# Kernel tuning notes

Hardware: AMD Instinct MI355X
Metric: run time of the kernel (lower is better)

Reference implementation:

```python
import jax, jax.numpy as jnp
import numpy as np


def _conv1x1(W, x):
    # W: [out, in], x: [B, in, D, H, W] -> [B, out, D, H, W]
    return jnp.einsum('oc,bcdhw->bodhw', W, x)


def _maxpool2(x):
    # 2x2x2 max pool, stride 2, over the last three (spatial) dims
    return jax.lax.reduce_window(x, -jnp.inf, jax.lax.max,
                                 (1, 1, 2, 2, 2), (1, 1, 2, 2, 2), 'VALID')


def setup_inputs() -> dict:
    key = jax.random.key(0)
    ks = jax.random.split(key, 5)
    B, C, D, H, W = 4, 256, 24, 24, 24
    Cq = C // 8
    x = jax.random.normal(ks[0], (B, C, D, H, W), dtype=jnp.float32)
    Wf = jax.random.normal(ks[1], (Cq, C), dtype=jnp.float32) * (C ** -0.5)
    Wg = jax.random.normal(ks[2], (Cq, C), dtype=jnp.float32) * (C ** -0.5)
    Wh = jax.random.normal(ks[3], (Cq, C), dtype=jnp.float32) * (C ** -0.5)
    Wv = jax.random.normal(ks[4], (C, Cq), dtype=jnp.float32) * (Cq ** -0.5)
    gamma = jnp.ones((), dtype=jnp.float32)
    return {"x": x, "Wf": Wf, "Wg": Wg, "Wh": Wh, "Wv": Wv, "gamma": gamma}


def reference(x, Wf, Wg, Wh, Wv, gamma):
    B, C, D, H, W = x.shape
    Cq = Wf.shape[0]
    N = D * H * W          # query length
    M = N // 8

    f = _conv1x1(Wf, x).reshape(B, Cq, N)                 # [B, Cq, N]
    g = _maxpool2(_conv1x1(Wg, x)).reshape(B, Cq, M)      # [B, Cq, M]
    h = _maxpool2(_conv1x1(Wh, x)).reshape(B, Cq, M)      # [B, Cq, M]

    scores = jnp.einsum('bcn,bcm->bnm', f, g)             # [B, N, M]
    beta = jax.nn.softmax(scores, axis=-1)
    o = jnp.einsum('bcm,bnm->bcn', h, beta)               # [B, Cq, N]
    o = _conv1x1(Wv, o.reshape(B, Cq, D, H, W))           # [B, C, D, H, W]
    return gamma * o + x
```

## Files before the change

### kernel.cpp

```cpp
#include <hip/hip_runtime.h>

#define B 4
#define C 256
#define CQ 32
#define NN 13824
#define MM 1728
#define MS 12

typedef __attribute__((ext_vector_type(8))) short short8;
typedef __attribute__((ext_vector_type(4))) float float4_;
typedef __attribute__((ext_vector_type(16))) float floatx16;

static __device__ inline unsigned rne_bf16(float x) {
  unsigned u = __float_as_uint(x);
  u += 0x7FFFu + ((u >> 16) & 1u);
  return u >> 16;
}

__global__ __launch_bounds__(256) void wcvt_kernel(
    const float* __restrict__ Wf, const float* __restrict__ Wg,
    const float* __restrict__ Wh, const float* __restrict__ Wv,
    unsigned short* __restrict__ W16c, unsigned short* __restrict__ Whv,
    unsigned short* __restrict__ Wlv) {
  const int i = blockIdx.x * 256 + threadIdx.x;
  if (i < 24576) {
    const int kk = i & 7;
    const int rest = i >> 3;
    const int m = rest % 96;
    const int r = rest / 96;
    const int kq = r & 3;
    const int ch = r >> 2;
    const int k = ch * 32 + kq * 8 + kk;
    const float* Wr = (m < 32) ? (Wf + m * C) : (m < 64) ? (Wg + (m - 32) * C)
                                                         : (Wh + (m - 64) * C);
    W16c[i] = (unsigned short)rne_bf16(Wr[k]);
  } else {
    const int j = i - 24576;
    const float v = Wv[j];
    const unsigned h = rne_bf16(v);
    Whv[j] = (unsigned short)h;
    Wlv[j] = (unsigned short)rne_bf16(v - __uint_as_float(h << 16));
  }
}

#define LOADX(SET, CH)                                                        \
  do {                                                                        \
    const float* xp = xbase + (size_t)((CH)*32) * NN;                         \
    _Pragma("unroll") for (int it = 0; it < 2; ++it) {                        \
      _Pragma("unroll") for (int kk = 0; kk < 8; ++kk)                        \
          vx[SET][it][kk] = xp[(size_t)((sh * 2 + it) * 8 + kk) * NN];        \
    }                                                                         \
  } while (0)

#define PACKX(SET, BUF)                                                       \
  do {                                                                        \
    _Pragma("unroll") for (int it = 0; it < 2; ++it) {                        \
      const int kq = sh * 2 + it;                                             \
      *reinterpret_cast<uint4*>(&xls[BUF][kq][sn][0]) = make_uint4(           \
          rne_bf16(vx[SET][it][0]) | (rne_bf16(vx[SET][it][1]) << 16),        \
          rne_bf16(vx[SET][it][2]) | (rne_bf16(vx[SET][it][3]) << 16),        \
          rne_bf16(vx[SET][it][4]) | (rne_bf16(vx[SET][it][5]) << 16),        \
          rne_bf16(vx[SET][it][6]) | (rne_bf16(vx[SET][it][7]) << 16));       \
    }                                                                         \
  } while (0)

#define LOADW(CH)                                                             \
  do {                                                                        \
    const uint4* src = reinterpret_cast<const uint4*>(W16c + (size_t)(CH)*3072); \
    wr0 = src[t];                                                             \
    if (t < 128) wr1 = src[256 + t];                                          \
  } while (0)

#define STOREW(BUF)                                                           \
  do {                                                                        \
    uint4* dst = reinterpret_cast<uint4*>(&wls[BUF][0][0][0]);                \
    dst[t] = wr0;                                                             \
    if (t < 128) dst[256 + t] = wr1;                                          \
  } while (0)

#define COMPUTE(BUF)                                                          \
  do {                                                                        \
    _Pragma("unroll") for (int ks = 0; ks < 2; ++ks) {                        \
      const int kq = ks * 2 + hi;                                             \
      const short8 bfr =                                                      \
          *reinterpret_cast<const short8*>(&xls[BUF][kq][w * 32 + col][0]);   \
      const short8 a0 = *reinterpret_cast<const short8*>(&wls[BUF][kq][col][0]);      \
      const short8 a1 = *reinterpret_cast<const short8*>(&wls[BUF][kq][32 + col][0]); \
      const short8 a2 = *reinterpret_cast<const short8*>(&wls[BUF][kq][64 + col][0]); \
      accf = __builtin_amdgcn_mfma_f32_32x32x16_bf16(a0, bfr, accf, 0, 0, 0); \
      accg = __builtin_amdgcn_mfma_f32_32x32x16_bf16(a1, bfr, accg, 0, 0, 0); \
      acch = __builtin_amdgcn_mfma_f32_32x32x16_bf16(a2, bfr, acch, 0, 0, 0); \
    }                                                                         \
  } while (0)

__global__ __launch_bounds__(256) void proj_mfma(
    const float* __restrict__ x, const unsigned short* __restrict__ W16c,
    unsigned short* __restrict__ f16, unsigned short* __restrict__ g16,
    unsigned short* __restrict__ h16) {
  __shared__ __align__(16) unsigned short xls[2][4][128][8];
  __shared__ __align__(16) unsigned short wls[2][4][96][8];
  const int blk = blockIdx.x;
  const int b = blk / 108;
  const int n0 = (blk - b * 108) * 128;
  const int t = threadIdx.x;
  const int w = t >> 6, lane = t & 63;
  const int col = lane & 31, hi = lane >> 5;
  const int sn = t & 127, sh = t >> 7;

  floatx16 accf = {0}, accg = {0}, acch = {0};
  const float* xbase = x + ((size_t)b * C) * NN + n0 + sn;
  float vx[2][2][8];
  uint4 wr0, wr1;

  LOADX(0, 0);
  PACKX(0, 0);
  LOADW(0);
  STOREW(0);
  LOADX(1, 1);
  __syncthreads();

#pragma unroll
  for (int ch = 0; ch < 8; ++ch) {
    const int buf = ch & 1;
    if (ch + 1 < 8) LOADW(ch + 1);
    if (ch + 2 < 8) {
      if (buf == 0) LOADX(0, ch + 2); else LOADX(1, ch + 2);
    }
    COMPUTE(buf);
    if (ch + 1 < 8) {
      if (buf == 0) PACKX(1, 1); else PACKX(0, 0);
      STOREW(buf ^ 1);
      __syncthreads();
    }
  }

  const int n = n0 + w * 32 + col;
  {
    unsigned short* fp = f16 + ((size_t)b * NN + n) * 32 + hi * 4;
#pragma unroll
    for (int rp = 0; rp < 8; ++rp) {
      const int m = (rp & 1) * 2 + 8 * (rp >> 1);
      *reinterpret_cast<unsigned*>(fp + m) =
          rne_bf16(accf[rp * 2]) | (rne_bf16(accf[rp * 2 + 1]) << 16);
    }
  }
  unsigned short* gp = g16 + (size_t)b * CQ * NN + n;
  unsigned short* hp = h16 + (size_t)b * CQ * NN + n;
#pragma unroll
  for (int r = 0; r < 16; ++r) {
    const int c = (r & 3) + 8 * (r >> 2) + 4 * hi;
    gp[(size_t)c * NN] = (unsigned short)rne_bf16(accg[r]);
    hp[(size_t)c * NN] = (unsigned short)rne_bf16(acch[r]);
  }
}

__global__ __launch_bounds__(256) void pool_kernel(
    const unsigned short* __restrict__ g16, const unsigned short* __restrict__ h16,
    unsigned short* __restrict__ gt16, unsigned short* __restrict__ ht16) {
  int i = blockIdx.x * 256 + threadIdx.x;
  const int c = i & 31;
  const int rest = i >> 5;
  const int m = rest % MM;
  const int b = rest / MM;
  const int wq = m % MS;
  const int hq = (m / MS) % MS;
  const int dq = m / (MS * MS);
  const size_t base = ((size_t)b * CQ + c) * NN +
                      (2 * dq) * 576 + (2 * hq) * 24 + (2 * wq);
  auto mx2 = [](unsigned u) {
    return fmaxf(__uint_as_float(u << 16), __uint_as_float(u & 0xFFFF0000u));
  };
  const unsigned short* pg = g16 + base;
  const unsigned short* ph = h16 + base;
  float vg = fmaxf(fmaxf(mx2(*(const unsigned*)(pg)),
                         mx2(*(const unsigned*)(pg + 24))),
                   fmaxf(mx2(*(const unsigned*)(pg + 576)),
                         mx2(*(const unsigned*)(pg + 600))));
  float vh = fmaxf(fmaxf(mx2(*(const unsigned*)(ph)),
                         mx2(*(const unsigned*)(ph + 24))),
                   fmaxf(mx2(*(const unsigned*)(ph + 576)),
                         mx2(*(const unsigned*)(ph + 600))));
  gt16[((size_t)b * MM + m) * 32 + c] = (unsigned short)(__float_as_uint(vg) >> 16);
  ht16[((size_t)b * 32 + c) * MM + m] = (unsigned short)(__float_as_uint(vh) >> 16);
}

__global__ __launch_bounds__(256, 4) void attn_kernel(
    const unsigned short* __restrict__ f16, const unsigned short* __restrict__ gt,
    const unsigned short* __restrict__ ht, const float* __restrict__ x,
    const unsigned short* __restrict__ Whv, const unsigned short* __restrict__ Wlv,
    const float* __restrict__ gamma, float* __restrict__ out) {
  __shared__ __align__(16) unsigned short sm[16896];
  const int blk = blockIdx.x;
  const int b = blk / 216;
  const int n0 = (blk - b * 216) * 64;
  const int t = threadIdx.x;
  const int w = t >> 6, L = t & 63, Q = L >> 4, col = L & 15;

  unsigned short* fls = sm;
  unsigned short* g0 = sm + 2560;
  unsigned short* g1 = sm + 5120;
  unsigned short* h0 = sm + 7680;
  unsigned short* h1 = sm + 9984;
  unsigned short* Pls = sm + 12288 + w * 1152;

  {
    const unsigned short* fsrc = f16 + ((size_t)(b * NN + n0)) * 32;
    *reinterpret_cast<uint4*>(fls + (t >> 2) * 40 + (t & 3) * 8) =
        *reinterpret_cast<const uint4*>(fsrc + t * 8);
  }
  const unsigned short* gsrc = gt + (size_t)b * MM * 32;
  const unsigned short* hsrc = ht + (size_t)b * 32 * MM;
  const int gk = t >> 2, gseg = t & 3;
  const int hc = t >> 3, hseg = t & 7;
  *reinterpret_cast<uint4*>(g0 + gk * 40 + gseg * 8) =
      *reinterpret_cast<const uint4*>(gsrc + gk * 32 + gseg * 8);
  *reinterpret_cast<uint4*>(h0 + hc * 72 + hseg * 8) =
      *reinterpret_cast<const uint4*>(hsrc + (size_t)hc * MM + hseg * 8);
  __syncthreads();

  const short8 fB = *reinterpret_cast<const short8*>(fls + (w * 16 + col) * 40 + Q * 8);

  float4_ acc0 = {0.f, 0.f, 0.f, 0.f}, acc1 = {0.f, 0.f, 0.f, 0.f};
  float l = 0.f;

  for (int ch = 0; ch < 27; ++ch) {
    unsigned short* gcur = (ch & 1) ? g1 : g0;
    unsigned short* hcur = (ch & 1) ? h1 : h0;
    uint4 gnx, hnx;
    if (ch < 26) {
      const int k0 = (ch + 1) * 64;
      gnx = *reinterpret_cast<const uint4*>(gsrc + (size_t)(k0 + gk) * 32 + gseg * 8);
      hnx = *reinterpret_cast<const uint4*>(hsrc + (size_t)hc * MM + k0 + hseg * 8);
    }
    float4_ sc[4];
#pragma unroll
    for (int T = 0; T < 4; ++T) {
      const short8 gA =
          *reinterpret_cast<const short8*>(gcur + (T * 16 + col) * 40 + Q * 8);
      float4_ z = {0.f, 0.f, 0.f, 0.f};
      sc[T] = __builtin_amdgcn_mfma_f32_16x16x32_bf16(gA, fB, z, 0, 0, 0);
    }
#pragma unroll
    for (int T = 0; T < 4; ++T) {
      const float p0 = __expf(sc[T][0] - 30.f);
      const float p1 = __expf(sc[T][1] - 30.f);
      const float p2 = __expf(sc[T][2] - 30.f);
      const float p3 = __expf(sc[T][3] - 30.f);
      l += (p0 + p1) + (p2 + p3);
      unsigned short* pw = Pls + col * 72 + T * 16 + Q * 4;
      *reinterpret_cast<uint2*>(pw) =
          make_uint2(rne_bf16(p0) | (rne_bf16(p1) << 16),
                     rne_bf16(p2) | (rne_bf16(p3) << 16));
    }
#pragma unroll
    for (int ks = 0; ks < 2; ++ks) {
      const short8 pA =
          *reinterpret_cast<const short8*>(Pls + col * 72 + ks * 32 + Q * 8);
      const short8 hB0 =
          *reinterpret_cast<const short8*>(hcur + col * 72 + ks * 32 + Q * 8);
      const short8 hB1 =
          *reinterpret_cast<const short8*>(hcur + (16 + col) * 72 + ks * 32 + Q * 8);
      acc0 = __builtin_amdgcn_mfma_f32_16x16x32_bf16(pA, hB0, acc0, 0, 0, 0);
      acc1 = __builtin_amdgcn_mfma_f32_16x16x32_bf16(pA, hB1, acc1, 0, 0, 0);
    }
    if (ch < 26) {
      unsigned short* gnb = (ch & 1) ? g0 : g1;
      unsigned short* hnb = (ch & 1) ? h0 : h1;
      *reinterpret_cast<uint4*>(gnb + gk * 40 + gseg * 8) = gnx;
      *reinterpret_cast<uint4*>(hnb + hc * 72 + hseg * 8) = hnx;
    }
    __syncthreads();
  }

  l += __shfl_xor(l, 16);
  l += __shfl_xor(l, 32);
  float* ols = reinterpret_cast<float*>(sm);
#pragma unroll
  for (int r = 0; r < 4; ++r) {
    const float linv = 1.f / __shfl(l, Q * 4 + r);
    const int nl = w * 16 + Q * 4 + r;
    ols[nl * 33 + col] = acc0[r] * linv;
    ols[nl * 33 + 16 + col] = acc1[r] * linv;
  }
  __syncthreads();

  const int colA = L & 31, hiA = L >> 5;
  const float gm = gamma[0];
  short8 Bf[2][2];
#pragma unroll
  for (int nt = 0; nt < 2; ++nt) {
#pragma unroll
    for (int ks = 0; ks < 2; ++ks) {
      const float* p = &ols[(nt * 32 + colA) * 33 + ks * 16 + hiA * 8];
      uint4 uu;
      uu.x = rne_bf16(p[0]) | (rne_bf16(p[1]) << 16);
      uu.y = rne_bf16(p[2]) | (rne_bf16(p[3]) << 16);
      uu.z = rne_bf16(p[4]) | (rne_bf16(p[5]) << 16);
      uu.w = rne_bf16(p[6]) | (rne_bf16(p[7]) << 16);
      Bf[nt][ks] = *reinterpret_cast<short8*>(&uu);
    }
  }
#pragma unroll
  for (int tt = 0; tt < 2; ++tt) {
    const int ct = w + tt * 4;
    const int ca = ct * 32 + colA;
    const short8 Ah0 = *reinterpret_cast<const short8*>(Whv + ca * 32 + hiA * 8);
    const short8 Ah1 = *reinterpret_cast<const short8*>(Whv + ca * 32 + 16 + hiA * 8);
    const short8 Al0 = *reinterpret_cast<const short8*>(Wlv + ca * 32 + hiA * 8);
    const short8 Al1 = *reinterpret_cast<const short8*>(Wlv + ca * 32 + 16 + hiA * 8);
    floatx16 ac0 = {0}, ac1 = {0};
    ac0 = __builtin_amdgcn_mfma_f32_32x32x16_bf16(Ah0, Bf[0][0], ac0, 0, 0, 0);
    ac0 = __builtin_amdgcn_mfma_f32_32x32x16_bf16(Ah1, Bf[0][1], ac0, 0, 0, 0);
    ac0 = __builtin_amdgcn_mfma_f32_32x32x16_bf16(Al0, Bf[0][0], ac0, 0, 0, 0);
    ac0 = __builtin_amdgcn_mfma_f32_32x32x16_bf16(Al1, Bf[0][1], ac0, 0, 0, 0);
    ac1 = __builtin_amdgcn_mfma_f32_32x32x16_bf16(Ah0, Bf[1][0], ac1, 0, 0, 0);
    ac1 = __builtin_amdgcn_mfma_f32_32x32x16_bf16(Ah1, Bf[1][1], ac1, 0, 0, 0);
    ac1 = __builtin_amdgcn_mfma_f32_32x32x16_bf16(Al0, Bf[1][0], ac1, 0, 0, 0);
    ac1 = __builtin_amdgcn_mfma_f32_32x32x16_bf16(Al1, Bf[1][1], ac1, 0, 0, 0);
#pragma unroll
    for (int nt = 0; nt < 2; ++nt) {
      const floatx16 av = nt ? ac1 : ac0;
      const int n = n0 + nt * 32 + colA;
      const float* xp = x + ((size_t)b * C + ct * 32 + 4 * hiA) * NN + n;
      float* op = out + ((size_t)b * C + ct * 32 + 4 * hiA) * NN + n;
      float xv[16];
#pragma unroll
      for (int r = 0; r < 16; ++r)
        xv[r] = xp[(size_t)((r & 3) + 8 * (r >> 2)) * NN];
#pragma unroll
      for (int r = 0; r < 16; ++r)
        op[(size_t)((r & 3) + 8 * (r >> 2)) * NN] = gm * av[r] + xv[r];
    }
  }
}

extern "C" void kernel_launch(void* const* d_in, const int* in_sizes, int n_in,
                              void* d_out, int out_size, void* d_ws, size_t ws_size,
                              hipStream_t stream) {
  const float* x     = (const float*)d_in[0];
  const float* Wf    = (const float*)d_in[1];
  const float* Wg    = (const float*)d_in[2];
  const float* Wh    = (const float*)d_in[3];
  const float* Wv    = (const float*)d_in[4];
  const float* gamma = (const float*)d_in[5];
  float* out = (float*)d_out;
  float* ws = (float*)d_ws;

  unsigned short* f16  = (unsigned short*)ws;
  unsigned short* g16  = (unsigned short*)(ws + 884736);
  unsigned short* h16  = (unsigned short*)(ws + 1769472);
  unsigned short* Whv  = (unsigned short*)(ws + 2654208);
  unsigned short* Wlv  = (unsigned short*)(ws + 2658304);
  unsigned short* gt16 = (unsigned short*)(ws + 4423680);
  unsigned short* ht16 = (unsigned short*)(ws + 4534272);
  unsigned short* W16c = (unsigned short*)(ws + 4644864);

  wcvt_kernel<<<128, 256, 0, stream>>>(Wf, Wg, Wh, Wv, W16c, Whv, Wlv);
  proj_mfma<<<B * 108, 256, 0, stream>>>(x, W16c, f16, g16, h16);
  pool_kernel<<<(B * CQ * MM) / 256, 256, 0, stream>>>(g16, h16, gt16, ht16);
  attn_kernel<<<B * (NN / 64), 256, 0, stream>>>(f16, gt16, ht16, x, Whv, Wlv,
                                                 gamma, out);
}
```

Measured before the change: 167.8 us.

## Read attention keys/values straight from global memory and deepen projection prefetch

The attention kernel no longer stages g and h tiles in shared memory with double buffering and per-chunk barriers. Each lane now loads its MFMA operands directly from global memory, relying on the cache, and sets wave priority around the MFMA blocks. Shared memory shrinks, which may allow more resident blocks, but operand loads are now uncoalesced and sit on the dependency chain. The projection kernel also prefetches x three chunks ahead instead of two, raising register use.

```diff
diff --git a/kernel.cpp b/kernel.cpp
--- a/kernel.cpp
+++ b/kernel.cpp
@@ -109,26 +109,25 @@
 
   floatx16 accf = {0}, accg = {0}, acch = {0};
   const float* xbase = x + ((size_t)b * C) * NN + n0 + sn;
-  float vx[2][2][8];
+  float vx[3][2][8];
   uint4 wr0, wr1;
 
   LOADX(0, 0);
+  LOADX(1, 1);
+  LOADX(2, 2);
+  LOADW(0);
   PACKX(0, 0);
-  LOADW(0);
   STOREW(0);
-  LOADX(1, 1);
   __syncthreads();
 
 #pragma unroll
   for (int ch = 0; ch < 8; ++ch) {
     const int buf = ch & 1;
     if (ch + 1 < 8) LOADW(ch + 1);
-    if (ch + 2 < 8) {
-      if (buf == 0) LOADX(0, ch + 2); else LOADX(1, ch + 2);
-    }
+    if (ch + 3 < 8) LOADX((ch + 3) % 3, ch + 3);
     COMPUTE(buf);
     if (ch + 1 < 8) {
-      if (buf == 0) PACKX(1, 1); else PACKX(0, 0);
+      PACKX((ch + 1) % 3, buf ^ 1);
       STOREW(buf ^ 1);
       __syncthreads();
     }
@@ -189,7 +188,7 @@
     const unsigned short* __restrict__ ht, const float* __restrict__ x,
     const unsigned short* __restrict__ Whv, const unsigned short* __restrict__ Wlv,
     const float* __restrict__ gamma, float* __restrict__ out) {
-  __shared__ __align__(16) unsigned short sm[16896];
+  __shared__ __align__(16) unsigned short sm[7168];
   const int blk = blockIdx.x;
   const int b = blk / 216;
   const int n0 = (blk - b * 216) * 64;
@@ -197,49 +196,35 @@
   const int w = t >> 6, L = t & 63, Q = L >> 4, col = L & 15;
 
   unsigned short* fls = sm;
-  unsigned short* g0 = sm + 2560;
-  unsigned short* g1 = sm + 5120;
-  unsigned short* h0 = sm + 7680;
-  unsigned short* h1 = sm + 9984;
-  unsigned short* Pls = sm + 12288 + w * 1152;
+  unsigned short* Pls = sm + 2560 + w * 1152;
 
   {
     const unsigned short* fsrc = f16 + ((size_t)(b * NN + n0)) * 32;
     *reinterpret_cast<uint4*>(fls + (t >> 2) * 40 + (t & 3) * 8) =
         *reinterpret_cast<const uint4*>(fsrc + t * 8);
   }
-  const unsigned short* gsrc = gt + (size_t)b * MM * 32;
-  const unsigned short* hsrc = ht + (size_t)b * 32 * MM;
-  const int gk = t >> 2, gseg = t & 3;
-  const int hc = t >> 3, hseg = t & 7;
-  *reinterpret_cast<uint4*>(g0 + gk * 40 + gseg * 8) =
-      *reinterpret_cast<const uint4*>(gsrc + gk * 32 + gseg * 8);
-  *reinterpret_cast<uint4*>(h0 + hc * 72 + hseg * 8) =
-      *reinterpret_cast<const uint4*>(hsrc + (size_t)hc * MM + hseg * 8);
   __syncthreads();
 
   const short8 fB = *reinterpret_cast<const short8*>(fls + (w * 16 + col) * 40 + Q * 8);
+
+  const unsigned short* gp0 = gt + ((size_t)b * MM + col) * 32 + Q * 8;
+  const unsigned short* hp0 = ht + ((size_t)b * 32 + col) * MM + Q * 8;
 
   float4_ acc0 = {0.f, 0.f, 0.f, 0.f}, acc1 = {0.f, 0.f, 0.f, 0.f};
   float l = 0.f;
 
   for (int ch = 0; ch < 27; ++ch) {
-    unsigned short* gcur = (ch & 1) ? g1 : g0;
-    unsigned short* hcur = (ch & 1) ? h1 : h0;
-    uint4 gnx, hnx;
-    if (ch < 26) {
-      const int k0 = (ch + 1) * 64;
-      gnx = *reinterpret_cast<const uint4*>(gsrc + (size_t)(k0 + gk) * 32 + gseg * 8);
-      hnx = *reinterpret_cast<const uint4*>(hsrc + (size_t)hc * MM + k0 + hseg * 8);
-    }
+    const int k0 = ch * 64;
     float4_ sc[4];
+    __builtin_amdgcn_s_setprio(1);
 #pragma unroll
     for (int T = 0; T < 4; ++T) {
       const short8 gA =
-          *reinterpret_cast<const short8*>(gcur + (T * 16 + col) * 40 + Q * 8);
+          *reinterpret_cast<const short8*>(gp0 + (size_t)(k0 + T * 16) * 32);
       float4_ z = {0.f, 0.f, 0.f, 0.f};
       sc[T] = __builtin_amdgcn_mfma_f32_16x16x32_bf16(gA, fB, z, 0, 0, 0);
     }
+    __builtin_amdgcn_s_setprio(0);
 #pragma unroll
     for (int T = 0; T < 4; ++T) {
       const float p0 = __expf(sc[T][0] - 30.f);
@@ -257,23 +242,19 @@
       const short8 pA =
           *reinterpret_cast<const short8*>(Pls + col * 72 + ks * 32 + Q * 8);
       const short8 hB0 =
-          *reinterpret_cast<const short8*>(hcur + col * 72 + ks * 32 + Q * 8);
+          *reinterpret_cast<const short8*>(hp0 + k0 + ks * 32);
       const short8 hB1 =
-          *reinterpret_cast<const short8*>(hcur + (16 + col) * 72 + ks * 32 + Q * 8);
+          *reinterpret_cast<const short8*>(hp0 + (size_t)16 * MM + k0 + ks * 32);
+      __builtin_amdgcn_s_setprio(1);
       acc0 = __builtin_amdgcn_mfma_f32_16x16x32_bf16(pA, hB0, acc0, 0, 0, 0);
       acc1 = __builtin_amdgcn_mfma_f32_16x16x32_bf16(pA, hB1, acc1, 0, 0, 0);
-    }
-    if (ch < 26) {
-      unsigned short* gnb = (ch & 1) ? g0 : g1;
-      unsigned short* hnb = (ch & 1) ? h0 : h1;
-      *reinterpret_cast<uint4*>(gnb + gk * 40 + gseg * 8) = gnx;
-      *reinterpret_cast<uint4*>(hnb + hc * 72 + hseg * 8) = hnx;
-    }
-    __syncthreads();
+      __builtin_amdgcn_s_setprio(0);
+    }
   }
 
   l += __shfl_xor(l, 16);
   l += __shfl_xor(l, 32);
+  __syncthreads();
   float* ols = reinterpret_cast<float*>(sm);
 #pragma unroll
   for (int r = 0; r < 4; ++r) {
```

Result: slower. 203.9 us (+21.5%).

## Vectorize x loads in projection, deepen prefetch, and reorder pool thread mapping

Applied to the files above, without the earlier changes.

The projection kernel now loads x as float4 along the spatial dimension, with each thread covering 4 positions by 4 channels, instead of scalar strided loads. It also widens register prefetch from two to three chunks ahead. The pool kernel's thread index mapping changes so neighbouring threads walk along the spatial index m rather than the channel, which should coalesce the g/h reads. The aim is fewer, wider global loads and better latency hiding, at the cost of more registers for the third prefetch set and narrower 8-byte LDS stores.

```diff
diff --git a/kernel.cpp b/kernel.cpp
--- a/kernel.cpp
+++ b/kernel.cpp
@@ -45,22 +45,20 @@
 
 #define LOADX(SET, CH)                                                        \
   do {                                                                        \
-    const float* xp = xbase + (size_t)((CH)*32) * NN;                         \
-    _Pragma("unroll") for (int it = 0; it < 2; ++it) {                        \
-      _Pragma("unroll") for (int kk = 0; kk < 8; ++kk)                        \
-          vx[SET][it][kk] = xp[(size_t)((sh * 2 + it) * 8 + kk) * NN];        \
-    }                                                                         \
+    const float* xp = xbase4 + (size_t)((CH)*32 + kg * 4) * NN;               \
+    _Pragma("unroll") for (int j = 0; j < 4; ++j)                             \
+        vx4[SET][j] = *reinterpret_cast<const float4*>(xp + (size_t)j * NN);  \
   } while (0)
 
 #define PACKX(SET, BUF)                                                       \
   do {                                                                        \
-    _Pragma("unroll") for (int it = 0; it < 2; ++it) {                        \
-      const int kq = sh * 2 + it;                                             \
-      *reinterpret_cast<uint4*>(&xls[BUF][kq][sn][0]) = make_uint4(           \
-          rne_bf16(vx[SET][it][0]) | (rne_bf16(vx[SET][it][1]) << 16),        \
-          rne_bf16(vx[SET][it][2]) | (rne_bf16(vx[SET][it][3]) << 16),        \
-          rne_bf16(vx[SET][it][4]) | (rne_bf16(vx[SET][it][5]) << 16),        \
-          rne_bf16(vx[SET][it][6]) | (rne_bf16(vx[SET][it][7]) << 16));       \
+    _Pragma("unroll") for (int i = 0; i < 4; ++i) {                           \
+      const unsigned u0 = rne_bf16(vx4[SET][0][i]) |                          \
+                          (rne_bf16(vx4[SET][1][i]) << 16);                   \
+      const unsigned u1 = rne_bf16(vx4[SET][2][i]) |                          \
+                          (rne_bf16(vx4[SET][3][i]) << 16);                   \
+      *reinterpret_cast<uint2*>(&xls[BUF][kg >> 1][nq * 4 + i][(kg & 1) * 4]) = \
+          make_uint2(u0, u1);                                                 \
     }                                                                         \
   } while (0)
 
@@ -105,30 +103,29 @@
   const int t = threadIdx.x;
   const int w = t >> 6, lane = t & 63;
   const int col = lane & 31, hi = lane >> 5;
-  const int sn = t & 127, sh = t >> 7;
+  const int nq = t & 31, kg = t >> 5;
 
   floatx16 accf = {0}, accg = {0}, acch = {0};
-  const float* xbase = x + ((size_t)b * C) * NN + n0 + sn;
-  float vx[2][2][8];
+  const float* xbase4 = x + ((size_t)b * C) * NN + n0 + nq * 4;
+  float4 vx4[3][4];
   uint4 wr0, wr1;
 
   LOADX(0, 0);
+  LOADX(1, 1);
+  LOADX(2, 2);
+  LOADW(0);
   PACKX(0, 0);
-  LOADW(0);
   STOREW(0);
-  LOADX(1, 1);
   __syncthreads();
 
 #pragma unroll
   for (int ch = 0; ch < 8; ++ch) {
     const int buf = ch & 1;
     if (ch + 1 < 8) LOADW(ch + 1);
-    if (ch + 2 < 8) {
-      if (buf == 0) LOADX(0, ch + 2); else LOADX(1, ch + 2);
-    }
+    if (ch + 3 < 8) LOADX((ch + 3) % 3, ch + 3);
     COMPUTE(buf);
     if (ch + 1 < 8) {
-      if (buf == 0) PACKX(1, 1); else PACKX(0, 0);
+      PACKX((ch + 1) % 3, buf ^ 1);
       STOREW(buf ^ 1);
       __syncthreads();
     }
@@ -158,10 +155,10 @@
     const unsigned short* __restrict__ g16, const unsigned short* __restrict__ h16,
     unsigned short* __restrict__ gt16, unsigned short* __restrict__ ht16) {
   int i = blockIdx.x * 256 + threadIdx.x;
-  const int c = i & 31;
-  const int rest = i >> 5;
-  const int m = rest % MM;
-  const int b = rest / MM;
+  const int m = i % MM;
+  const int rest = i / MM;
+  const int c = rest & 31;
+  const int b = rest >> 5;
   const int wq = m % MS;
   const int hq = (m / MS) % MS;
   const int dq = m / (MS * MS);
```

Result: no change. 165.6 us (-1.3%).
